# Kernel optimization log

Measured on AMD Instinct MI355X. Metric: run time of the kernel, lower is better.

## Reference

```python
import jax, jax.numpy as jnp
import numpy as np

# pywt db8 decomposition low-pass filter (dec_lo), 16 taps
DB8_DEC_LO = np.array([
    -0.00011747678400228192, 0.0006754494059985568, -0.0003917403729959771,
    -0.00487035299301066, 0.008746094047015655, 0.013981027917015516,
    -0.04408825393106472, -0.01736930100202211, 0.128747426620186,
    0.00047248457399797254, -0.2840155429624281, -0.015829105256023893,
    0.5853546836548691, 0.6756307362980128, 0.3128715909144659,
    0.05441584224308161], dtype=np.float32)
FLEN = 16
_signs = ((-1.0) ** np.arange(FLEN)).astype(np.float32)
DEC_LO = jnp.asarray(DB8_DEC_LO)
REC_LO = DEC_LO[::-1]                      # rec_lo = reversed dec_lo
REC_HI = jnp.asarray(DB8_DEC_LO * _signs)  # rec_hi[n] = (-1)^n dec_lo[n]
DEC_HI = REC_HI[::-1]                      # dec_hi = reversed rec_hi
DN = ('NCH', 'OIH', 'NCH')


def _dwt_db8(x):
    """pywt.dwt(x, 'db8', mode='symmetric') along last axis. x: [N, T]."""
    ext = jnp.pad(x, ((0, 0), (FLEN - 1, FLEN - 1)), mode='symmetric')
    # true convolution (filter flipped), downsample starting at index 1
    k = jnp.stack([DEC_LO[::-1], DEC_HI[::-1]])[:, None, :]  # [2,1,FLEN]
    y = jax.lax.conv_general_dilated(ext[:, None, 1:], k, (2,), 'VALID',
                                     dimension_numbers=DN)   # [N,2,c]
    return y[:, 0], y[:, 1]


def _idwt_db8(ca, cd, out_len):
    """pywt.idwt(ca, cd, 'db8') -> [N, out_len]; out_len = 2*c - FLEN + 2."""
    n, c = ca.shape
    up = jnp.zeros((n, 2, 2 * c), ca.dtype)
    up = up.at[:, 0, 1::2].set(ca).at[:, 1, 1::2].set(cd)  # zero-interleave
    k = jnp.stack([REC_LO[::-1], REC_HI[::-1]])[None]      # [1,2,FLEN]
    y = jax.lax.conv_general_dilated(up, k, (1,), ((FLEN - 1, FLEN - 1),),
                                     dimension_numbers=DN)  # full conv
    return y[:, 0, FLEN - 1: FLEN - 1 + out_len]


def setup_inputs() -> dict:
    key = jax.random.key(0)
    k1, k2 = jax.random.split(key)
    x_in = jax.random.normal(k1, (32, 4096, 512), dtype=jnp.float32)
    threshold_param = jax.random.uniform(k2, (1,), dtype=jnp.float32) * 0.5
    return {"x_in": x_in, "threshold_param": threshold_param}


def reference(x_in, threshold_param):
    B, T, C = x_in.shape
    x = jnp.transpose(x_in.astype(jnp.float32), (0, 2, 1)).reshape(B * C, T)
    low, high = _dwt_db8(x)                    # [B*C, W] each
    W = high.shape[-1]
    high_bcw = high.reshape(B, C, W)
    high_s = high_bcw ** 2
    # torch.quantile(high_s, q(1,), dim=-1, keepdim=True) -> (1,B,C,1) -> view (B,C,1)
    threshold = jnp.quantile(high_s, threshold_param, axis=-1,
                             keepdims=True).reshape(B, C, 1)
    adaptive_mask = (high_s > threshold).astype(high_s.dtype)
    high_masked = (high_bcw * adaptive_mask).reshape(B * C, W)
    rec = _idwt_db8(low, high_masked, T)       # [B*C, T]
    return rec.reshape(B, C, T).transpose(0, 2, 1)
```

## Files before the change

### kernel.cpp

```cpp
#include <hip/hip_runtime.h>
#include <stdint.h>

#define T_LEN 4096
#define C_LEN 512
#define B_LEN 32
#define W_LEN 2055
#define NCH 16
#define HPITCH 2057
#define XPITCH 21
#define LPITCH 17
#define NCHUNK1 33
#define NCHUNK3 32
#define LO_ROWS 2056

typedef float f32x4 __attribute__((ext_vector_type(4)));

__device__ __constant__ float c_dec_lo[16] = {
    (float)-0.00011747678400228192, (float)0.0006754494059985568,
    (float)-0.0003917403729959771,  (float)-0.00487035299301066,
    (float)0.008746094047015655,    (float)0.013981027917015516,
    (float)-0.04408825393106472,    (float)-0.01736930100202211,
    (float)0.128747426620186,       (float)0.00047248457399797254,
    (float)-0.2840155429624281,     (float)-0.015829105256023893,
    (float)0.5853546836548691,      (float)0.6756307362980128,
    (float)0.3128715909144659,      (float)0.05441584224308161};

__device__ __forceinline__ int sym_idx(int j) {
  int t = j - 15;
  if (t < 0) t = -1 - t;
  if (t >= T_LEN) t = 2 * T_LEN - 1 - t;
  return t;
}

__global__ __launch_bounds__(1024) void k_fused(const float* __restrict__ x,
                                                const float* __restrict__ qp,
                                                float* __restrict__ lo_ws,
                                                float* __restrict__ out) {
  __shared__ float hi_lds[NCH * HPITCH];
  __shared__ __align__(16) uint32_t hist[NCH * 256];
  __shared__ float stage[142 * XPITCH];
  __shared__ float s_thr[NCH];

  const int o = blockIdx.x;
  const int blk = (o & 7) * 128 + (o >> 3);
  const int b = blk >> 5;
  const int c0 = (blk & 31) * NCH;
  const int tid = threadIdx.x;
  float* lo_blk = lo_ws + (size_t)blk * (LO_ROWS * NCH);
  const size_t xrow = (size_t)b * T_LEN;

  const int cth = tid & 15;
  const int wl = tid >> 4;

  const int s_jj0 = tid >> 4;
  const int s_jj1 = s_jj0 + 64;
  const int s_jj2 = s_jj0 + 128;
  const bool has2 = (tid < 224);

  float pa, pb, pc;
  {
    const int jbase = 1;
    pa = x[(xrow + sym_idx(jbase + s_jj0)) * C_LEN + c0 + cth];
    pb = x[(xrow + sym_idx(jbase + s_jj1)) * C_LEN + c0 + cth];
    if (has2) pc = x[(xrow + sym_idx(jbase + s_jj2)) * C_LEN + c0 + cth];
  }

  for (int ci = 0; ci < NCHUNK1; ++ci) {
    __syncthreads();
    stage[s_jj0 * XPITCH + cth] = pa;
    stage[s_jj1 * XPITCH + cth] = pb;
    if (has2) stage[s_jj2 * XPITCH + cth] = pc;
    __syncthreads();
    if (ci + 1 < NCHUNK1) {
      const int jbase = 128 * (ci + 1) + 1;
      pa = x[(xrow + sym_idx(jbase + s_jj0)) * C_LEN + c0 + cth];
      pb = x[(xrow + sym_idx(jbase + s_jj1)) * C_LEN + c0 + cth];
      if (has2) pc = x[(xrow + sym_idx(jbase + s_jj2)) * C_LEN + c0 + cth];
    }
    const int w = 64 * ci + wl;
    if (w < W_LEN) {
      float accl = 0.f, acch = 0.f;
#pragma unroll
      for (int u = 0; u < 16; ++u) {
        float e = stage[(2 * wl + 15 - u) * XPITCH + cth];
        accl = fmaf(c_dec_lo[u], e, accl);
        float dh = (u & 1) ? c_dec_lo[15 - u] : -c_dec_lo[15 - u];
        acch = fmaf(dh, e, acch);
      }
      hi_lds[cth * HPITCH + w] = acch;
      lo_blk[w * NCH + cth] = accl;
    }
  }
  __syncthreads();

  const float q = qp[0];
  float pos = __fmul_rn(q, (float)(W_LEN - 1));
  if (pos < 0.f) pos = 0.f;
  if (pos > (float)(W_LEN - 1)) pos = (float)(W_LEN - 1);
  const int lo_i = (int)floorf(pos);
  const int hi_i = (int)ceilf(pos);
  const float gwt = pos - floorf(pos);
  const float lwt = 1.0f - gwt;

  const int ch = tid >> 6;
  const int ln = tid & 63;
  uint32_t* hh = hist + ch * 256;
  const float* hrow = hi_lds + ch * HPITCH;

  int kk = lo_i;
  uint32_t pref = 0;
  const uint32_t pmask[4] = {0u, 0xFF000000u, 0xFFFF0000u, 0xFFFFFF00u};
#pragma unroll
  for (int p = 0; p < 4; ++p) {
    const int shift = 24 - 8 * p;
    {
      uint4 z = {0u, 0u, 0u, 0u};
      *(uint4*)(hh + 4 * ln) = z;
    }
    __syncthreads();
    for (int i = ln; i < W_LEN; i += 64) {
      float v = hrow[i];
      uint32_t key = __float_as_uint(__fmul_rn(v, v));
      if ((key & pmask[p]) == (pref & pmask[p]))
        atomicAdd(&hh[(key >> shift) & 255u], 1u);
    }
    __syncthreads();
    uint4 cc = *(const uint4*)(hh + 4 * ln);
    const uint32_t sum4 = cc.x + cc.y + cc.z + cc.w;
    uint32_t incl = sum4;
#pragma unroll
    for (int d = 1; d < 64; d <<= 1) {
      uint32_t v = (uint32_t)__shfl_up((int)incl, d);
      if (ln >= d) incl += v;
    }
    const uint32_t excl = incl - sum4;
    const bool has = ((uint32_t)kk >= excl) && ((uint32_t)kk < excl + sum4);
    int k2 = kk - (int)excl;
    int bsel = 0;
    if (has) {
      if (k2 >= (int)cc.x) {
        k2 -= (int)cc.x;
        bsel = 1;
        if (k2 >= (int)cc.y) {
          k2 -= (int)cc.y;
          bsel = 2;
          if (k2 >= (int)cc.z) {
            k2 -= (int)cc.z;
            bsel = 3;
          }
        }
      }
    }
    const unsigned long long mvote = __ballot(has ? 1 : 0);
    const int src = __ffsll(mvote) - 1;
    const int binv = __shfl(4 * ln + bsel, src);
    kk = __shfl(k2, src);
    pref |= ((uint32_t)binv) << shift;
    __syncthreads();
  }
  const float a_lo = __uint_as_float(pref);

  float a_hi_v;
  if (hi_i == lo_i) {
    a_hi_v = a_lo;
  } else {
    int cnt = 0;
    uint32_t mn = 0xFFFFFFFFu;
    for (int i = ln; i < W_LEN; i += 64) {
      float v = hrow[i];
      uint32_t key = __float_as_uint(__fmul_rn(v, v));
      if (key <= pref)
        cnt++;
      else
        mn = mn < key ? mn : key;
    }
#pragma unroll
    for (int d = 1; d < 64; d <<= 1) {
      cnt += __shfl_xor(cnt, d);
      uint32_t om = (uint32_t)__shfl_xor((int)mn, d);
      mn = mn < om ? mn : om;
    }
    a_hi_v = (cnt >= lo_i + 2) ? a_lo : __uint_as_float(mn);
  }
  if (ln == 0)
    s_thr[ch] = __fadd_rn(__fmul_rn(a_lo, lwt), __fmul_rn(a_hi_v, gwt));
  __syncthreads();

  for (int cc2 = 0; cc2 < NCH; ++cc2) {
    const float th = s_thr[cc2];
    for (int i = tid; i < W_LEN; i += 1024) {
      float v = hi_lds[cc2 * HPITCH + i];
      hi_lds[cc2 * HPITCH + i] = (__fmul_rn(v, v) > th) ? v : 0.f;
    }
  }
  __syncthreads();

  const bool ldr = (tid < 288);
  const int g = tid >> 4;
  f32x4 pf;
  if (ldr) pf = *(const f32x4*)(lo_blk + (size_t)tid * 4);

  for (int cs = 0; cs < NCHUNK3; ++cs) {
    __syncthreads();
    if (ldr) {
      const int wloc = tid >> 2;
      const int cc4 = (tid & 3) * 4;
      const int bse = wloc * LPITCH + cc4;
      stage[bse + 0] = pf.x;
      stage[bse + 1] = pf.y;
      stage[bse + 2] = pf.z;
      stage[bse + 3] = pf.w;
    }
    __syncthreads();
    if (ldr && cs + 1 < NCHUNK3)
      pf = *(const f32x4*)(lo_blk + (size_t)(cs + 1) * 1024 + (size_t)tid * 4);

    float acc0 = 0.f, acc1 = 0.f;
    const int mg = 64 * cs;
#pragma unroll
    for (int j = 0; j < 8; ++j) {
      const int ml = g + 7 - j;
      const float ca = stage[ml * LPITCH + cth];
      const float cd = hi_lds[cth * HPITCH + mg + ml];
      const int u0 = 2 * j;
      acc0 = fmaf(c_dec_lo[u0], cd, fmaf(c_dec_lo[15 - u0], ca, acc0));
      const int u1 = 2 * j + 1;
      acc1 = fmaf(-c_dec_lo[u1], cd, fmaf(c_dec_lo[15 - u1], ca, acc1));
    }
    const size_t ob = (xrow + 128 * cs + 2 * g) * C_LEN + c0 + cth;
    __builtin_nontemporal_store(acc0, out + ob);
    __builtin_nontemporal_store(acc1, out + ob + C_LEN);
  }
}

extern "C" void kernel_launch(void* const* d_in, const int* in_sizes, int n_in,
                              void* d_out, int out_size, void* d_ws,
                              size_t ws_size, hipStream_t stream) {
  const float* x = (const float*)d_in[0];
  const float* qp = (const float*)d_in[1];
  float* out = (float*)d_out;
  float* lo_ws = (float*)d_ws;

  k_fused<<<dim3(B_LEN * (C_LEN / NCH)), dim3(1024), 0, stream>>>(x, qp, lo_ws,
                                                                  out);
}
```

Baseline: 623.4 us.

## Register-block DWT/IDWT per thread and cache quantile keys in registers

The forward DWT now has each thread compute 8 consecutive outputs from a 30-element register window loaded straight from global memory, replacing the LDS staging loop and its barriers. The radix-select threshold search keeps each lane's 33 squared keys in registers and drops the per-pass barriers, since each wavefront owns one channel's histogram. The inverse DWT computes 8 outputs per thread from register windows of lo and hi coefficients, removing staging and barriers. The aim is less LDS traffic and synchronisation, at the cost of heavier register pressure that may reduce occupancy, redundant overlapping global loads, and reliance on wavefront-level ordering for histogram correctness.

```diff
diff --git a/kernel.cpp b/kernel.cpp
--- a/kernel.cpp
+++ b/kernel.cpp
@@ -7,13 +7,7 @@
 #define W_LEN 2055
 #define NCH 16
 #define HPITCH 2057
-#define XPITCH 21
-#define LPITCH 17
-#define NCHUNK1 33
-#define NCHUNK3 32
 #define LO_ROWS 2056
-
-typedef float f32x4 __attribute__((ext_vector_type(4)));
 
 __device__ __constant__ float c_dec_lo[16] = {
     (float)-0.00011747678400228192, (float)0.0006754494059985568,
@@ -38,8 +32,6 @@
                                                 float* __restrict__ out) {
   __shared__ float hi_lds[NCH * HPITCH];
   __shared__ __align__(16) uint32_t hist[NCH * 256];
-  __shared__ float stage[142 * XPITCH];
-  __shared__ float s_thr[NCH];
 
   const int o = blockIdx.x;
   const int blk = (o & 7) * 128 + (o >> 3);
@@ -52,44 +44,45 @@
   const int cth = tid & 15;
   const int wl = tid >> 4;
 
-  const int s_jj0 = tid >> 4;
-  const int s_jj1 = s_jj0 + 64;
-  const int s_jj2 = s_jj0 + 128;
-  const bool has2 = (tid < 224);
-
-  float pa, pb, pc;
-  {
-    const int jbase = 1;
-    pa = x[(xrow + sym_idx(jbase + s_jj0)) * C_LEN + c0 + cth];
-    pb = x[(xrow + sym_idx(jbase + s_jj1)) * C_LEN + c0 + cth];
-    if (has2) pc = x[(xrow + sym_idx(jbase + s_jj2)) * C_LEN + c0 + cth];
-  }
-
-  for (int ci = 0; ci < NCHUNK1; ++ci) {
-    __syncthreads();
-    stage[s_jj0 * XPITCH + cth] = pa;
-    stage[s_jj1 * XPITCH + cth] = pb;
-    if (has2) stage[s_jj2 * XPITCH + cth] = pc;
-    __syncthreads();
-    if (ci + 1 < NCHUNK1) {
-      const int jbase = 128 * (ci + 1) + 1;
-      pa = x[(xrow + sym_idx(jbase + s_jj0)) * C_LEN + c0 + cth];
-      pb = x[(xrow + sym_idx(jbase + s_jj1)) * C_LEN + c0 + cth];
-      if (has2) pc = x[(xrow + sym_idx(jbase + s_jj2)) * C_LEN + c0 + cth];
-    }
-    const int w = 64 * ci + wl;
-    if (w < W_LEN) {
+  const float* xc = x + xrow * C_LEN + c0 + cth;
+#pragma unroll
+  for (int m = 0; m < 4; ++m) {
+    const int wb = 8 * wl + 512 * m;
+    float E[30];
+    if (wb == 0) {
+#pragma unroll
+      for (int i = 0; i < 30; ++i) E[i] = xc[(size_t)sym_idx(1 + i) * C_LEN];
+    } else {
+      const float* p = xc + (size_t)(2 * wb - 14) * C_LEN;
+#pragma unroll
+      for (int i = 0; i < 30; ++i) E[i] = p[(size_t)i * C_LEN];
+    }
+#pragma unroll
+    for (int k = 0; k < 8; ++k) {
       float accl = 0.f, acch = 0.f;
 #pragma unroll
       for (int u = 0; u < 16; ++u) {
-        float e = stage[(2 * wl + 15 - u) * XPITCH + cth];
+        float e = E[2 * k + 15 - u];
         accl = fmaf(c_dec_lo[u], e, accl);
         float dh = (u & 1) ? c_dec_lo[15 - u] : -c_dec_lo[15 - u];
         acch = fmaf(dh, e, acch);
       }
-      hi_lds[cth * HPITCH + w] = acch;
-      lo_blk[w * NCH + cth] = accl;
-    }
+      hi_lds[cth * HPITCH + wb + k] = acch;
+      lo_blk[(wb + k) * NCH + cth] = accl;
+    }
+  }
+  if (wl < 7) {
+    const int w = 2048 + wl;
+    float accl = 0.f, acch = 0.f;
+#pragma unroll
+    for (int u = 0; u < 16; ++u) {
+      float e = xc[(size_t)sym_idx(2 * w + 16 - u) * C_LEN];
+      accl = fmaf(c_dec_lo[u], e, accl);
+      float dh = (u & 1) ? c_dec_lo[15 - u] : -c_dec_lo[15 - u];
+      acch = fmaf(dh, e, acch);
+    }
+    hi_lds[cth * HPITCH + w] = acch;
+    lo_blk[w * NCH + cth] = accl;
   }
   __syncthreads();
 
@@ -104,27 +97,38 @@
 
   const int ch = tid >> 6;
   const int ln = tid & 63;
+  const float* hrow = hi_lds + ch * HPITCH;
   uint32_t* hh = hist + ch * 256;
-  const float* hrow = hi_lds + ch * HPITCH;
+
+  uint32_t key[33];
+#pragma unroll
+  for (int m = 0; m < 32; ++m) {
+    float v = hrow[ln + 64 * m];
+    key[m] = __float_as_uint(__fmul_rn(v, v));
+  }
+  if (ln < 7) {
+    float v = hrow[2048 + ln];
+    key[32] = __float_as_uint(__fmul_rn(v, v));
+  } else {
+    key[32] = 0xFFFFFFFFu;
+  }
 
   int kk = lo_i;
   uint32_t pref = 0;
-  const uint32_t pmask[4] = {0u, 0xFF000000u, 0xFFFF0000u, 0xFFFFFF00u};
+  const int shs[4] = {23, 15, 7, 0};
 #pragma unroll
   for (int p = 0; p < 4; ++p) {
-    const int shift = 24 - 8 * p;
+    const int sh = shs[p];
     {
       uint4 z = {0u, 0u, 0u, 0u};
       *(uint4*)(hh + 4 * ln) = z;
     }
-    __syncthreads();
-    for (int i = ln; i < W_LEN; i += 64) {
-      float v = hrow[i];
-      uint32_t key = __float_as_uint(__fmul_rn(v, v));
-      if ((key & pmask[p]) == (pref & pmask[p]))
-        atomicAdd(&hh[(key >> shift) & 255u], 1u);
-    }
-    __syncthreads();
+    const uint32_t pc = pref >> (sh + 8);
+#pragma unroll
+    for (int m = 0; m < 33; ++m) {
+      if ((key[m] >> (sh + 8)) == pc)
+        atomicAdd(&hh[(key[m] >> sh) & 255u], 1u);
+    }
     uint4 cc = *(const uint4*)(hh + 4 * ln);
     const uint32_t sum4 = cc.x + cc.y + cc.z + cc.w;
     uint32_t incl = sum4;
@@ -151,12 +155,11 @@
         }
       }
     }
-    const unsigned long long mvote = __ballot(has ? 1 : 0);
-    const int src = __ffsll(mvote) - 1;
+    const unsigned long long mv = __ballot(has ? 1 : 0);
+    const int src = __ffsll(mv) - 1;
     const int binv = __shfl(4 * ln + bsel, src);
     kk = __shfl(k2, src);
-    pref |= ((uint32_t)binv) << shift;
-    __syncthreads();
+    pref |= ((uint32_t)binv) << sh;
   }
   const float a_lo = __uint_as_float(pref);
 
@@ -166,13 +169,15 @@
   } else {
     int cnt = 0;
     uint32_t mn = 0xFFFFFFFFu;
-    for (int i = ln; i < W_LEN; i += 64) {
-      float v = hrow[i];
-      uint32_t key = __float_as_uint(__fmul_rn(v, v));
-      if (key <= pref)
-        cnt++;
-      else
-        mn = mn < key ? mn : key;
+#pragma unroll
+    for (int m = 0; m < 33; ++m) {
+      bool valid = (m < 32) || (ln < 7);
+      if (valid) {
+        if (key[m] <= pref)
+          cnt++;
+        else
+          mn = mn < key[m] ? mn : key[m];
+      }
     }
 #pragma unroll
     for (int d = 1; d < 64; d <<= 1) {
@@ -182,54 +187,48 @@
     }
     a_hi_v = (cnt >= lo_i + 2) ? a_lo : __uint_as_float(mn);
   }
-  if (ln == 0)
-    s_thr[ch] = __fadd_rn(__fmul_rn(a_lo, lwt), __fmul_rn(a_hi_v, gwt));
+  const float th = __fadd_rn(__fmul_rn(a_lo, lwt), __fmul_rn(a_hi_v, gwt));
+
+#pragma unroll
+  for (int m = 0; m < 32; ++m) {
+    if (!(__uint_as_float(key[m]) > th)) hi_lds[ch * HPITCH + ln + 64 * m] = 0.f;
+  }
+  if (ln < 7) {
+    if (!(__uint_as_float(key[32]) > th)) hi_lds[ch * HPITCH + 2048 + ln] = 0.f;
+  }
   __syncthreads();
 
-  for (int cc2 = 0; cc2 < NCH; ++cc2) {
-    const float th = s_thr[cc2];
-    for (int i = tid; i < W_LEN; i += 1024) {
-      float v = hi_lds[cc2 * HPITCH + i];
-      hi_lds[cc2 * HPITCH + i] = (__fmul_rn(v, v) > th) ? v : 0.f;
-    }
-  }
-  __syncthreads();
-
-  const bool ldr = (tid < 288);
-  const int g = tid >> 4;
-  f32x4 pf;
-  if (ldr) pf = *(const f32x4*)(lo_blk + (size_t)tid * 4);
-
-  for (int cs = 0; cs < NCHUNK3; ++cs) {
-    __syncthreads();
-    if (ldr) {
-      const int wloc = tid >> 2;
-      const int cc4 = (tid & 3) * 4;
-      const int bse = wloc * LPITCH + cc4;
-      stage[bse + 0] = pf.x;
-      stage[bse + 1] = pf.y;
-      stage[bse + 2] = pf.z;
-      stage[bse + 3] = pf.w;
-    }
-    __syncthreads();
-    if (ldr && cs + 1 < NCHUNK3)
-      pf = *(const f32x4*)(lo_blk + (size_t)(cs + 1) * 1024 + (size_t)tid * 4);
-
-    float acc0 = 0.f, acc1 = 0.f;
-    const int mg = 64 * cs;
-#pragma unroll
-    for (int j = 0; j < 8; ++j) {
-      const int ml = g + 7 - j;
-      const float ca = stage[ml * LPITCH + cth];
-      const float cd = hi_lds[cth * HPITCH + mg + ml];
-      const int u0 = 2 * j;
-      acc0 = fmaf(c_dec_lo[u0], cd, fmaf(c_dec_lo[15 - u0], ca, acc0));
-      const int u1 = 2 * j + 1;
-      acc1 = fmaf(-c_dec_lo[u1], cd, fmaf(c_dec_lo[15 - u1], ca, acc1));
-    }
-    const size_t ob = (xrow + 128 * cs + 2 * g) * C_LEN + c0 + cth;
-    __builtin_nontemporal_store(acc0, out + ob);
-    __builtin_nontemporal_store(acc1, out + ob + C_LEN);
+#pragma unroll
+  for (int m2 = 0; m2 < 8; ++m2) {
+    const int sg = wl + 64 * m2;
+    const int mb = 4 * sg;
+    float A[11], D[11];
+#pragma unroll
+    for (int i = 0; i < 11; ++i) A[i] = lo_blk[(mb + i) * NCH + cth];
+#pragma unroll
+    for (int i = 0; i < 11; ++i) D[i] = hi_lds[cth * HPITCH + mb + i];
+    const size_t ob = (xrow + 8 * sg) * C_LEN + c0 + cth;
+#pragma unroll
+    for (int k = 0; k < 8; ++k) {
+      float acc = 0.f;
+      const int q2 = k >> 1;
+      if ((k & 1) == 0) {
+#pragma unroll
+        for (int j = 0; j < 8; ++j) {
+          const int u = 2 * j;
+          const int li = q2 + 7 - j;
+          acc = fmaf(c_dec_lo[u], D[li], fmaf(c_dec_lo[15 - u], A[li], acc));
+        }
+      } else {
+#pragma unroll
+        for (int j = 0; j < 8; ++j) {
+          const int u = 2 * j + 1;
+          const int li = q2 + 7 - j;
+          acc = fmaf(-c_dec_lo[u], D[li], fmaf(c_dec_lo[15 - u], A[li], acc));
+        }
+      }
+      __builtin_nontemporal_store(acc, out + ob + (size_t)k * C_LEN);
+    }
   }
 }
 
```

New measurement: 553.5 us. -11.2%, faster.
